# Optimization experiments

Hardware: AMD Instinct MI355X
Metric: run time of the kernel (lower is better)

The kernel has to match this reference:

```python
import jax, jax.numpy as jnp
import numpy as np

B, S, D = 2, 2048, 2048
HQ, HKV = 32, 8
DH = D // HQ  # 64
NUM_REP = HQ // HKV  # 4


def setup_inputs() -> dict:
    key = jax.random.key(0)
    k1, k2, k3, k4, k5 = jax.random.split(key, 5)
    scale = 0.02
    return {
        "x": jax.random.normal(k1, (B, S, D), dtype=jnp.float32),
        "Wq": jax.random.normal(k2, (D, HQ * DH), dtype=jnp.float32) * scale,
        "Wk": jax.random.normal(k3, (D, HKV * DH), dtype=jnp.float32) * scale,
        "Wv": jax.random.normal(k4, (D, HKV * DH), dtype=jnp.float32) * scale,
        "Wo": jax.random.normal(k5, (HQ * DH, D), dtype=jnp.float32) * scale,
    }


def reference(x, Wq, Wk, Wv, Wo):
    b, s, _ = x.shape
    # projections
    xq = (x @ Wq).reshape(b, s, HQ, DH)    # [B,S,HQ,DH]
    xk = (x @ Wk).reshape(b, s, HKV, DH)   # [B,S,HKV,DH]
    xv = (x @ Wv).reshape(b, s, HKV, DH)
    # repeat kv heads to match query heads (GQA expand)
    keys = jnp.repeat(xk, NUM_REP, axis=2)    # [B,S,HQ,DH]
    values = jnp.repeat(xv, NUM_REP, axis=2)
    # scores: [B,HQ,S,S], fp32 softmax (no causal mask in original)
    scores = jnp.einsum("bqhd,bkhd->bhqk", xq, keys) / jnp.sqrt(jnp.float32(DH))
    probs = jax.nn.softmax(scores.astype(jnp.float32), axis=-1).astype(xq.dtype)
    context = jnp.einsum("bhqk,bkhd->bqhd", probs, values)  # [B,S,HQ,DH]
    context = context.reshape(b, s, HQ * DH)
    return context @ Wo
```

## Files before the change

kernel.cpp:

```cpp
#include <hip/hip_runtime.h>
#include <cstdint>
#include <cstddef>
#include <cmath>

typedef __bf16 bf16x8 __attribute__((ext_vector_type(8)));
typedef float  f32x4  __attribute__((ext_vector_type(4)));
typedef unsigned short us4 __attribute__((ext_vector_type(4)));

__device__ __forceinline__ unsigned short f2bf(float f) {
    union { float f; unsigned int u; } v; v.f = f;
    unsigned int u = v.u;
    u += 0x7fffu + ((u >> 16) & 1u);
    return (unsigned short)(u >> 16);
}

__device__ __forceinline__ unsigned int fbits(float f) {
    union { float f; unsigned int u; } v; v.f = f; return v.u;
}

__device__ __forceinline__ unsigned int pk_bf16_trunc(float a, float b) {
    return __builtin_amdgcn_perm(fbits(b), fbits(a), 0x07060302u);
}

__device__ __forceinline__ void gld_lds16(const void* g, void* l) {
    __builtin_amdgcn_global_load_lds((__attribute__((address_space(1))) void*)g,
                                     (__attribute__((address_space(3))) void*)l,
                                     16, 0, 0);
}

#define BB   2
#define SS   2048
#define DD   2048
#define HQ   32
#define HKV  8
#define DH   64
#define MM   (BB * SS)
#define NQKV 3072

#define QSCALE 0.18033688011112042f

__global__ __launch_bounds__(256) void cast_f32_bf16(const float* __restrict__ src,
                                                     unsigned short* __restrict__ dst,
                                                     int n) {
    int i = (blockIdx.x * 256 + threadIdx.x) * 4;
    if (i >= n) return;
    const float4 f = *(const float4*)(src + i);
    us4 o;
    o[0] = f2bf(f.x); o[1] = f2bf(f.y); o[2] = f2bf(f.z); o[3] = f2bf(f.w);
    *(us4*)(dst + i) = o;
}

__global__ __launch_bounds__(256) void transpose_cast2(const float* __restrict__ srcA,
                                                       const float* __restrict__ srcB,
                                                       unsigned short* __restrict__ dstA,
                                                       unsigned short* __restrict__ dstB,
                                                       int R, int C,
                                                       float sA, float sB) {
    __shared__ __attribute__((aligned(16))) float tile[32][33];
    const float* src = blockIdx.z ? srcB : srcA;
    unsigned short* dst = blockIdx.z ? dstB : dstA;
    const float scl = blockIdx.z ? sB : sA;
    const int c0 = blockIdx.x * 32, r0 = blockIdx.y * 32;
    const int tx = threadIdx.x & 31, ty = threadIdx.x >> 5;
    #pragma unroll
    for (int dy = 0; dy < 32; dy += 8)
        tile[ty + dy][tx] = src[(size_t)(r0 + ty + dy) * C + c0 + tx];
    __syncthreads();
    #pragma unroll
    for (int dy = 0; dy < 32; dy += 8)
        dst[(size_t)(c0 + ty + dy) * R + r0 + tx] = f2bf(tile[tx][ty + dy] * scl);
}

__global__ __launch_bounds__(256) void transpose_v(const unsigned short* __restrict__ qkv,
                                                   unsigned short* __restrict__ vt) {
    __shared__ __attribute__((aligned(16))) unsigned short tile[32][33];
    const int s0 = blockIdx.x * 32, d0 = blockIdx.y * 32;
    const int bh = blockIdx.z;
    const int b = bh >> 3, kvh = bh & 7;
    const int tx = threadIdx.x & 31, ty = threadIdx.x >> 5;
    #pragma unroll
    for (int dy = 0; dy < 32; dy += 8)
        tile[ty + dy][tx] =
            qkv[(size_t)(b * SS + s0 + ty + dy) * NQKV + 2560 + kvh * DH + d0 + tx];
    __syncthreads();
    #pragma unroll
    for (int dy = 0; dy < 32; dy += 8)
        vt[(size_t)((b * HKV + kvh) * DH + d0 + ty + dy) * SS + s0 + tx] =
            tile[tx][ty + dy];
}

template <int OUT_BF16>
__global__ __launch_bounds__(256) void gemm_bt(const unsigned short* __restrict__ A,
                                               const unsigned short* __restrict__ Bt,
                                               void* __restrict__ Cout,
                                               int M, int N, int K) {
    __shared__ __attribute__((aligned(16))) unsigned short As[128 * 64];
    __shared__ __attribute__((aligned(16))) unsigned short Bs[128 * 64];
    const int bm = blockIdx.x, bn = blockIdx.y;
    const int tid = threadIdx.x;
    const int wave = tid >> 6, lane = tid & 63;
    const int wm = (wave >> 1) * 64, wn = (wave & 1) * 64;
    const int g = lane >> 4, l15 = lane & 15;
    const int sr = lane >> 3;
    const int sc8 = ((lane & 7) ^ (sr & 7)) * 8;
    const int r7 = l15 & 7;

    f32x4 acc[4][4] = {};
    const unsigned short* aBase = A  + (size_t)(bm * 128) * K;
    const unsigned short* bBase = Bt + (size_t)(bn * 128) * K;

    for (int kt = 0; kt < K; kt += 64) {
        __syncthreads();
        #pragma unroll
        for (int j = 0; j < 4; ++j) {
            const int i = wave * 4 + j;
            gld_lds16(aBase + (size_t)(i * 8 + sr) * K + kt + sc8, &As[i * 512]);
            gld_lds16(bBase + (size_t)(i * 8 + sr) * K + kt + sc8, &Bs[i * 512]);
        }
        __syncthreads();
        #pragma unroll
        for (int ks = 0; ks < 2; ++ks) {
            bf16x8 af[4], bfr[4];
            #pragma unroll
            for (int t = 0; t < 4; ++t) {
                af[t]  = *(const bf16x8*)&As[(wm + t * 16 + l15) * 64 + ((ks * 4 + g) ^ r7) * 8];
                bfr[t] = *(const bf16x8*)&Bs[(wn + t * 16 + l15) * 64 + ((ks * 4 + g) ^ r7) * 8];
            }
            #pragma unroll
            for (int i = 0; i < 4; ++i)
                #pragma unroll
                for (int j = 0; j < 4; ++j)
                    acc[i][j] = __builtin_amdgcn_mfma_f32_16x16x32_bf16(
                        af[i], bfr[j], acc[i][j], 0, 0, 0);
        }
    }
    #pragma unroll
    for (int i = 0; i < 4; ++i) {
        #pragma unroll
        for (int j = 0; j < 4; ++j) {
            const int col = bn * 128 + wn + j * 16 + l15;
            #pragma unroll
            for (int r = 0; r < 4; ++r) {
                const int row = bm * 128 + wm + i * 16 + g * 4 + r;
                const float v = acc[i][j][r];
                if (OUT_BF16)
                    ((unsigned short*)Cout)[(size_t)row * N + col] = f2bf(v);
                else
                    ((float*)Cout)[(size_t)row * N + col] = v;
            }
        }
    }
}

__global__ __launch_bounds__(256, 4) void flash_attn(const unsigned short* __restrict__ qkv,
                                                     const unsigned short* __restrict__ vt,
                                                     unsigned short* __restrict__ ctx) {
    __shared__ __attribute__((aligned(16))) unsigned short Ks[2][64 * 64];
    __shared__ __attribute__((aligned(16))) unsigned short Vs[2][64 * 64];

    const int qt = blockIdx.x, h = blockIdx.y, b = blockIdx.z;
    const int kvh = h >> 2;
    const int tid = threadIdx.x, wave = tid >> 6, lane = tid & 63;
    const int g = lane >> 4, l15 = lane & 15;
    const int sr = lane >> 3;
    const int sc8 = ((lane & 7) ^ (sr & 7)) * 8;
    const int r7 = l15 & 7;
    const int qb = qt * 128 + wave * 32;

    const unsigned short* kbase = qkv + (size_t)(b * SS) * NQKV + 2048 + kvh * DH;
    const unsigned short* vbase = vt + (size_t)((b * HKV + kvh) * DH) * SS;

    bf16x8 qf[2][2];
    #pragma unroll
    for (int n = 0; n < 2; ++n)
        #pragma unroll
        for (int kh = 0; kh < 2; ++kh)
            qf[n][kh] = *(const bf16x8*)(qkv +
                (size_t)(b * SS + qb + n * 16 + l15) * NQKV + h * DH + kh * 32 + g * 8);

    bf16x8 ones;
    #pragma unroll
    for (int i = 0; i < 8; ++i) ones[i] = (__bf16)1.0f;

    const unsigned short* sp[4];
    size_t sadv;
    if (wave < 2) {
        #pragma unroll
        for (int j = 0; j < 4; ++j) {
            const int rho = (wave * 4 + j) * 8 + sr;
            const int key = (rho & 0x23) | ((rho & 0x0C) << 1) | ((rho & 0x10) >> 2);
            sp[j] = kbase + (size_t)key * NQKV + sc8;
        }
        sadv = (size_t)64 * NQKV;
    } else {
        #pragma unroll
        for (int j = 0; j < 4; ++j)
            sp[j] = vbase + (size_t)(((wave - 2) * 4 + j) * 8 + sr) * SS + sc8;
        sadv = 64;
    }

    #define STAGE(buf)                                                        \
        do {                                                                  \
            if (wave < 2) {                                                   \
                _Pragma("unroll")                                             \
                for (int j = 0; j < 4; ++j)                                   \
                    gld_lds16(sp[j], &Ks[buf][(wave * 4 + j) * 512]);         \
            } else {                                                          \
                _Pragma("unroll")                                             \
                for (int j = 0; j < 4; ++j)                                   \
                    gld_lds16(sp[j], &Vs[buf][((wave - 2) * 4 + j) * 512]);   \
            }                                                                 \
            _Pragma("unroll")                                                 \
            for (int j = 0; j < 4; ++j) sp[j] += sadv;                        \
        } while (0)

    f32x4 oacc[2][4] = {};
    f32x4 lacc[2] = {};

    STAGE(0);
    int cur = 0;

    for (int kt = 0; kt < SS; kt += 64) {
        __syncthreads();
        if (kt + 64 < SS) { STAGE(cur ^ 1); }

        const unsigned short* ks = Ks[cur];
        const unsigned short* vs = Vs[cur];

        #pragma unroll
        for (int p = 0; p < 2; ++p) {
            uint4 pk4[2];
            #pragma unroll
            for (int hh = 0; hh < 2; ++hh) {
                const int t = 2 * p + hh;
                bf16x8 kf0 = *(const bf16x8*)&ks[(t * 16 + l15) * 64 + ((g) ^ r7) * 8];
                bf16x8 kf1 = *(const bf16x8*)&ks[(t * 16 + l15) * 64 + ((4 + g) ^ r7) * 8];
                #pragma unroll
                for (int n = 0; n < 2; ++n) {
                    f32x4 c = {};
                    c = __builtin_amdgcn_mfma_f32_16x16x32_bf16(kf0, qf[n][0], c, 0, 0, 0);
                    c = __builtin_amdgcn_mfma_f32_16x16x32_bf16(kf1, qf[n][1], c, 0, 0, 0);
                    f32x4 pe;
                    pe[0] = __builtin_amdgcn_exp2f(c[0]);
                    pe[1] = __builtin_amdgcn_exp2f(c[1]);
                    pe[2] = __builtin_amdgcn_exp2f(c[2]);
                    pe[3] = __builtin_amdgcn_exp2f(c[3]);
                    const unsigned int lo = pk_bf16_trunc(pe[0], pe[1]);
                    const unsigned int hi = pk_bf16_trunc(pe[2], pe[3]);
                    if (hh == 0) { pk4[n].x = lo; pk4[n].y = hi; }
                    else         { pk4[n].z = lo; pk4[n].w = hi; }
                }
            }
            __builtin_amdgcn_s_setprio(1);
            #pragma unroll
            for (int nt = 0; nt < 4; ++nt) {
                bf16x8 vf = *(const bf16x8*)&vs[(nt * 16 + l15) * 64 +
                                                (((p << 2) + g) ^ r7) * 8];
                #pragma unroll
                for (int m = 0; m < 2; ++m) {
                    union { uint4 u; bf16x8 v; } pa; pa.u = pk4[m];
                    oacc[m][nt] = __builtin_amdgcn_mfma_f32_16x16x32_bf16(
                        pa.v, vf, oacc[m][nt], 0, 0, 0);
                    if (nt == 0)
                        lacc[m] = __builtin_amdgcn_mfma_f32_16x16x32_bf16(
                            pa.v, ones, lacc[m], 0, 0, 0);
                }
            }
            __builtin_amdgcn_s_setprio(0);
        }
        cur ^= 1;
    }

    #pragma unroll
    for (int m = 0; m < 2; ++m) {
        #pragma unroll
        for (int r = 0; r < 4; ++r) {
            const float inv = 1.0f / lacc[m][r];
            const int token = b * SS + qb + m * 16 + g * 4 + r;
            #pragma unroll
            for (int nt = 0; nt < 4; ++nt)
                ctx[(size_t)token * (HQ * DH) + h * DH + nt * 16 + l15] =
                    f2bf(oacc[m][nt][r] * inv);
        }
    }
    #undef STAGE
}

extern "C" void kernel_launch(void* const* d_in, const int* in_sizes, int n_in,
                              void* d_out, int out_size, void* d_ws, size_t ws_size,
                              hipStream_t stream) {
    (void)in_sizes; (void)n_in; (void)out_size; (void)ws_size;
    const float* x  = (const float*)d_in[0];
    const float* Wq = (const float*)d_in[1];
    const float* Wk = (const float*)d_in[2];
    const float* Wv = (const float*)d_in[3];
    const float* Wo = (const float*)d_in[4];
    float* out = (float*)d_out;

    char* ws = (char*)d_ws;
    unsigned short* xb     = (unsigned short*)(ws);
    unsigned short* WqkvT  = (unsigned short*)(ws + 16777216);
    unsigned short* WoT    = (unsigned short*)(ws + 29360128);
    unsigned short* QKV    = (unsigned short*)(ws + 37748736);
    unsigned short* Vt     = (unsigned short*)(ws + 62914560);
    unsigned short* ctx    = (unsigned short*)(ws + 67108864);

    cast_f32_bf16<<<8192, 256, 0, stream>>>(x, xb, MM * DD);
    transpose_cast2<<<dim3(64, 64, 2), 256, 0, stream>>>(Wq, Wo, WqkvT, WoT, 2048, 2048,
                                                         QSCALE, 1.0f);
    transpose_cast2<<<dim3(16, 64, 2), 256, 0, stream>>>(
        Wk, Wv, WqkvT + (size_t)2048 * 2048, WqkvT + (size_t)2560 * 2048, 2048, 512,
        1.0f, 1.0f);

    gemm_bt<1><<<dim3(32, 24), 256, 0, stream>>>(xb, WqkvT, QKV, MM, NQKV, DD);

    transpose_v<<<dim3(64, 2, 16), 256, 0, stream>>>(QKV, Vt);

    flash_attn<<<dim3(16, 32, 2), 256, 0, stream>>>(QKV, Vt, ctx);

    gemm_bt<0><<<dim3(32, 16), 256, 0, stream>>>(ctx, WoT, out, MM, DD, DD);
}
```

Measured before the change: 290.8 us.

## Merge prep kernels into one launch and manually unroll attention double-buffer loop

Folds the x cast and the three weight transpose-casts into a single prep kernel that dispatches on block index, replacing three launches with one. In flash attention, the K/V tile loop is unrolled by two with constant buffer indices, so the buffer toggle and its dynamic indexing go away. The score MFMA now starts from a zero constant, and the final normalisation uses a hardware reciprocal instead of a divide. The gain from saving two launches is small, and the rcp approximation changes rounding slightly.

```diff
diff --git a/kernel.cpp b/kernel.cpp
--- a/kernel.cpp
+++ b/kernel.cpp
@@ -39,28 +39,37 @@
 
 #define QSCALE 0.18033688011112042f
 
-__global__ __launch_bounds__(256) void cast_f32_bf16(const float* __restrict__ src,
-                                                     unsigned short* __restrict__ dst,
-                                                     int n) {
-    int i = (blockIdx.x * 256 + threadIdx.x) * 4;
-    if (i >= n) return;
-    const float4 f = *(const float4*)(src + i);
-    us4 o;
-    o[0] = f2bf(f.x); o[1] = f2bf(f.y); o[2] = f2bf(f.z); o[3] = f2bf(f.w);
-    *(us4*)(dst + i) = o;
-}
-
-__global__ __launch_bounds__(256) void transpose_cast2(const float* __restrict__ srcA,
-                                                       const float* __restrict__ srcB,
-                                                       unsigned short* __restrict__ dstA,
-                                                       unsigned short* __restrict__ dstB,
-                                                       int R, int C,
-                                                       float sA, float sB) {
+__global__ __launch_bounds__(256) void prep(const float* __restrict__ x,
+                                            const float* __restrict__ Wq,
+                                            const float* __restrict__ Wk,
+                                            const float* __restrict__ Wv,
+                                            const float* __restrict__ Wo,
+                                            unsigned short* __restrict__ xb,
+                                            unsigned short* __restrict__ WqkvT,
+                                            unsigned short* __restrict__ WoT) {
+    const int bid = blockIdx.x;
+    if (bid < 8192) {
+        const int i = (bid * 256 + threadIdx.x) * 4;
+        const float4 f = *(const float4*)(x + i);
+        us4 o;
+        o[0] = f2bf(f.x); o[1] = f2bf(f.y); o[2] = f2bf(f.z); o[3] = f2bf(f.w);
+        *(us4*)(xb + i) = o;
+        return;
+    }
+    const float* src; unsigned short* dst; int C, bx, by; float scl = 1.0f;
+    int r = bid - 8192;
+    if (r < 4096) {
+        src = Wq; dst = WqkvT; C = 2048; bx = r & 63; by = r >> 6; scl = QSCALE;
+    } else if (r < 8192) {
+        r -= 4096; src = Wo; dst = WoT; C = 2048; bx = r & 63; by = r >> 6;
+    } else if (r < 9216) {
+        r -= 8192; src = Wk; dst = WqkvT + (size_t)2048 * 2048; C = 512; bx = r & 15; by = r >> 4;
+    } else {
+        r -= 9216; src = Wv; dst = WqkvT + (size_t)2560 * 2048; C = 512; bx = r & 15; by = r >> 4;
+    }
+    const int R = 2048;
     __shared__ __attribute__((aligned(16))) float tile[32][33];
-    const float* src = blockIdx.z ? srcB : srcA;
-    unsigned short* dst = blockIdx.z ? dstB : dstA;
-    const float scl = blockIdx.z ? sB : sA;
-    const int c0 = blockIdx.x * 32, r0 = blockIdx.y * 32;
+    const int c0 = bx * 32, r0 = by * 32;
     const int tx = threadIdx.x & 31, ty = threadIdx.x >> 5;
     #pragma unroll
     for (int dy = 0; dy < 32; dy += 8)
@@ -182,6 +191,8 @@
     #pragma unroll
     for (int i = 0; i < 8; ++i) ones[i] = (__bf16)1.0f;
 
+    const f32x4 z4 = {0.0f, 0.0f, 0.0f, 0.0f};
+
     const unsigned short* sp[4];
     size_t sadv;
     if (wave < 2) {
@@ -217,65 +228,71 @@
     f32x4 oacc[2][4] = {};
     f32x4 lacc[2] = {};
 
+    #define TILE(BUF)                                                                          \
+        do {                                                                                   \
+            const unsigned short* ks = Ks[BUF];                                                \
+            const unsigned short* vs = Vs[BUF];                                                \
+            _Pragma("unroll")                                                                  \
+            for (int p = 0; p < 2; ++p) {                                                      \
+                uint4 pk4[2];                                                                  \
+                _Pragma("unroll")                                                              \
+                for (int hh = 0; hh < 2; ++hh) {                                               \
+                    const int t = 2 * p + hh;                                                  \
+                    bf16x8 kf0 = *(const bf16x8*)&ks[(t * 16 + l15) * 64 + ((g) ^ r7) * 8];    \
+                    bf16x8 kf1 = *(const bf16x8*)&ks[(t * 16 + l15) * 64 + ((4 + g) ^ r7) * 8];\
+                    _Pragma("unroll")                                                          \
+                    for (int n = 0; n < 2; ++n) {                                              \
+                        f32x4 c = __builtin_amdgcn_mfma_f32_16x16x32_bf16(                     \
+                            kf0, qf[n][0], z4, 0, 0, 0);                                       \
+                        c = __builtin_amdgcn_mfma_f32_16x16x32_bf16(                           \
+                            kf1, qf[n][1], c, 0, 0, 0);                                        \
+                        f32x4 pe;                                                              \
+                        pe[0] = __builtin_amdgcn_exp2f(c[0]);                                  \
+                        pe[1] = __builtin_amdgcn_exp2f(c[1]);                                  \
+                        pe[2] = __builtin_amdgcn_exp2f(c[2]);                                  \
+                        pe[3] = __builtin_amdgcn_exp2f(c[3]);                                  \
+                        const unsigned int lo = pk_bf16_trunc(pe[0], pe[1]);                   \
+                        const unsigned int hi = pk_bf16_trunc(pe[2], pe[3]);                   \
+                        if (hh == 0) { pk4[n].x = lo; pk4[n].y = hi; }                         \
+                        else         { pk4[n].z = lo; pk4[n].w = hi; }                         \
+                    }                                                                          \
+                }                                                                              \
+                __builtin_amdgcn_s_setprio(1);                                                 \
+                _Pragma("unroll")                                                              \
+                for (int nt = 0; nt < 4; ++nt) {                                               \
+                    bf16x8 vf = *(const bf16x8*)&vs[(nt * 16 + l15) * 64 +                     \
+                                                    (((p << 2) + g) ^ r7) * 8];                \
+                    _Pragma("unroll")                                                          \
+                    for (int m = 0; m < 2; ++m) {                                              \
+                        union { uint4 u; bf16x8 v; } pa; pa.u = pk4[m];                        \
+                        oacc[m][nt] = __builtin_amdgcn_mfma_f32_16x16x32_bf16(                 \
+                            pa.v, vf, oacc[m][nt], 0, 0, 0);                                   \
+                        if (nt == 0)                                                           \
+                            lacc[m] = __builtin_amdgcn_mfma_f32_16x16x32_bf16(                 \
+                                pa.v, ones, lacc[m], 0, 0, 0);                                 \
+                    }                                                                          \
+                }                                                                              \
+                __builtin_amdgcn_s_setprio(0);                                                 \
+            }                                                                                  \
+        } while (0)
+
     STAGE(0);
-    int cur = 0;
-
-    for (int kt = 0; kt < SS; kt += 64) {
+
+    #pragma unroll 1
+    for (int kt2 = 0; kt2 < 16; ++kt2) {
         __syncthreads();
-        if (kt + 64 < SS) { STAGE(cur ^ 1); }
-
-        const unsigned short* ks = Ks[cur];
-        const unsigned short* vs = Vs[cur];
-
-        #pragma unroll
-        for (int p = 0; p < 2; ++p) {
-            uint4 pk4[2];
-            #pragma unroll
-            for (int hh = 0; hh < 2; ++hh) {
-                const int t = 2 * p + hh;
-                bf16x8 kf0 = *(const bf16x8*)&ks[(t * 16 + l15) * 64 + ((g) ^ r7) * 8];
-                bf16x8 kf1 = *(const bf16x8*)&ks[(t * 16 + l15) * 64 + ((4 + g) ^ r7) * 8];
-                #pragma unroll
-                for (int n = 0; n < 2; ++n) {
-                    f32x4 c = {};
-                    c = __builtin_amdgcn_mfma_f32_16x16x32_bf16(kf0, qf[n][0], c, 0, 0, 0);
-                    c = __builtin_amdgcn_mfma_f32_16x16x32_bf16(kf1, qf[n][1], c, 0, 0, 0);
-                    f32x4 pe;
-                    pe[0] = __builtin_amdgcn_exp2f(c[0]);
-                    pe[1] = __builtin_amdgcn_exp2f(c[1]);
-                    pe[2] = __builtin_amdgcn_exp2f(c[2]);
-                    pe[3] = __builtin_amdgcn_exp2f(c[3]);
-                    const unsigned int lo = pk_bf16_trunc(pe[0], pe[1]);
-                    const unsigned int hi = pk_bf16_trunc(pe[2], pe[3]);
-                    if (hh == 0) { pk4[n].x = lo; pk4[n].y = hi; }
-                    else         { pk4[n].z = lo; pk4[n].w = hi; }
-                }
-            }
-            __builtin_amdgcn_s_setprio(1);
-            #pragma unroll
-            for (int nt = 0; nt < 4; ++nt) {
-                bf16x8 vf = *(const bf16x8*)&vs[(nt * 16 + l15) * 64 +
-                                                (((p << 2) + g) ^ r7) * 8];
-                #pragma unroll
-                for (int m = 0; m < 2; ++m) {
-                    union { uint4 u; bf16x8 v; } pa; pa.u = pk4[m];
-                    oacc[m][nt] = __builtin_amdgcn_mfma_f32_16x16x32_bf16(
-                        pa.v, vf, oacc[m][nt], 0, 0, 0);
-                    if (nt == 0)
-                        lacc[m] = __builtin_amdgcn_mfma_f32_16x16x32_bf16(
-                            pa.v, ones, lacc[m], 0, 0, 0);
-                }
-            }
-            __builtin_amdgcn_s_setprio(0);
-        }
-        cur ^= 1;
+        STAGE(1);
+        TILE(0);
+        __syncthreads();
+        if (kt2 < 15) STAGE(0);
+        TILE(1);
     }
 
     #pragma unroll
     for (int m = 0; m < 2; ++m) {
         #pragma unroll
         for (int r = 0; r < 4; ++r) {
-            const float inv = 1.0f / lacc[m][r];
+            const float inv = __builtin_amdgcn_rcpf(lacc[m][r]);
             const int token = b * SS + qb + m * 16 + g * 4 + r;
             #pragma unroll
             for (int nt = 0; nt < 4; ++nt)
@@ -283,6 +300,7 @@
                     f2bf(oacc[m][nt][r] * inv);
         }
     }
+    #undef TILE
     #undef STAGE
 }
 
@@ -305,12 +323,7 @@
     unsigned short* Vt     = (unsigned short*)(ws + 62914560);
     unsigned short* ctx    = (unsigned short*)(ws + 67108864);
 
-    cast_f32_bf16<<<8192, 256, 0, stream>>>(x, xb, MM * DD);
-    transpose_cast2<<<dim3(64, 64, 2), 256, 0, stream>>>(Wq, Wo, WqkvT, WoT, 2048, 2048,
-                                                         QSCALE, 1.0f);
-    transpose_cast2<<<dim3(16, 64, 2), 256, 0, stream>>>(
-        Wk, Wv, WqkvT + (size_t)2048 * 2048, WqkvT + (size_t)2560 * 2048, 2048, 512,
-        1.0f, 1.0f);
+    prep<<<18432, 256, 0, stream>>>(x, Wq, Wk, Wv, Wo, xb, WqkvT, WoT);
 
     gemm_bt<1><<<dim3(32, 24), 256, 0, stream>>>(xb, WqkvT, QKV, MM, NQKV, DD);
 
```

Measured after the change: 287.2 us. Within noise of the previous version (-1.2%).
